# Optimization experiments

Hardware: AMD Instinct MI355X
Metric: run time of the kernel (lower is better)

## Reference

```python
import jax, jax.numpy as jnp
import numpy as np

IMG, P, CIN, D, K, L, H, FF, B = 512, 32, 3, 256, 8192, 6, 8, 1024, 32
GRID = IMG // P  # 16
DH = D // H
EPS = 1e-5


def _ln(x, w, b):
    m = x.mean(-1, keepdims=True)
    v = ((x - m) ** 2).mean(-1, keepdims=True)
    return (x - m) / jnp.sqrt(v + EPS) * w + b


def _mha(x, wqkv, bqkv, wo, bo):
    # x: (S, Bt, D) -- axis 0 is the attention axis (torch batch_first=False quirk)
    S, Bt, _ = x.shape
    qkv = x @ wqkv.T + bqkv
    q, k, v = jnp.split(qkv, 3, axis=-1)
    q = q.reshape(S, Bt, H, DH)
    k = k.reshape(S, Bt, H, DH)
    v = v.reshape(S, Bt, H, DH)
    scores = jnp.einsum('sbhd,tbhd->bhst', q, k) / jnp.sqrt(jnp.float32(DH))
    attn = jax.nn.softmax(scores, axis=-1)
    o = jnp.einsum('bhst,tbhd->sbhd', attn, v).reshape(S, Bt, D)
    return o @ wo.T + bo


def _conv_t(x, w, b, stride=2, pad=1):
    # w uses torch ConvTranspose2d layout (Cin, Cout, kH, kW)
    kH = w.shape[2]
    wf = jnp.flip(w, (2, 3)).transpose(1, 0, 2, 3)  # -> (Cout, Cin, kH, kW)
    y = jax.lax.conv_general_dilated(
        x, wf, window_strides=(1, 1),
        padding=[(kH - 1 - pad, kH - 1 - pad)] * 2,
        lhs_dilation=(stride, stride),
        dimension_numbers=('NCHW', 'OIHW', 'NCHW'))
    return y + b[None, :, None, None]


def _forward(x, patch_w, patch_b, qkv_w, qkv_b, out_w, out_b, ln1_w, ln1_b,
             ln2_w, ln2_b, ff1_w, ff1_b, ff2_w, ff2_b, lnf_w, lnf_b, codebook,
             dec_w0, dec_b0, dec_w1, dec_b1, dec_w2, dec_b2, dec_w3, dec_b3):
    # patch embedding: conv stride=patch -> (B, D, G, G) -> (B, N, D)
    h = jax.lax.conv_general_dilated(
        x, patch_w, (P, P), 'VALID',
        dimension_numbers=('NCHW', 'OIHW', 'NCHW')) + patch_b[None, :, None, None]
    h = h.reshape(h.shape[0], D, -1).transpose(0, 2, 1)  # (B, N, D)
    # torch TransformerEncoderLayer default batch_first=False: attention runs
    # over axis 0 (image batch); faithfully replicated here. Post-norm, eval
    # mode (dropout=identity), exact gelu.
    for i in range(L):
        a = _mha(h, qkv_w[i], qkv_b[i], out_w[i], out_b[i])
        h = _ln(h + a, ln1_w[i], ln1_b[i])
        f = jax.nn.gelu(h @ ff1_w[i].T + ff1_b[i], approximate=False) @ ff2_w[i].T + ff2_b[i]
        h = _ln(h + f, ln2_w[i], ln2_b[i])
    h = _ln(h, lnf_w, lnf_b)
    # vector quantization: squared-distance argmin over codebook
    flat = h.reshape(-1, D)  # (B*N, D)
    d = ((flat ** 2).sum(-1, keepdims=True)
         - 2.0 * flat @ codebook.T
         + (codebook ** 2).sum(-1))  # (B*N, K)
    idx = jnp.argmin(d, axis=1)
    q = codebook[idx].reshape(h.shape)
    e_loss = jnp.mean((jax.lax.stop_gradient(q) - h) ** 2)
    q_loss = jnp.mean((q - jax.lax.stop_gradient(h)) ** 2)
    vq_loss = q_loss + 0.25 * e_loss
    q = h + jax.lax.stop_gradient(q - h)  # straight-through
    q = q.transpose(0, 2, 1).reshape(x.shape[0], D, GRID, GRID)
    y = jax.nn.relu(_conv_t(q, dec_w0, dec_b0))
    y = jax.nn.relu(_conv_t(y, dec_w1, dec_b1))
    y = jax.nn.relu(_conv_t(y, dec_w2, dec_b2))
    x_hat = jax.nn.sigmoid(_conv_t(y, dec_w3, dec_b3))
    return x_hat, vq_loss


def setup_inputs() -> dict:
    key = jax.random.key(0)
    ks = iter(jax.random.split(key, 64))
    nrm = lambda shape, s=0.02: jax.random.normal(next(ks), shape, jnp.float32) * s
    f32 = jnp.float32
    return {
        'x': jax.random.normal(next(ks), (B, CIN, IMG, IMG), f32),
        'patch_w': nrm((D, CIN, P, P)),
        'patch_b': jnp.zeros((D,), f32),
        'qkv_w': nrm((L, 3 * D, D)),
        'qkv_b': jnp.zeros((L, 3 * D), f32),
        'out_w': nrm((L, D, D)),
        'out_b': jnp.zeros((L, D), f32),
        'ln1_w': jnp.ones((L, D), f32),
        'ln1_b': jnp.zeros((L, D), f32),
        'ln2_w': jnp.ones((L, D), f32),
        'ln2_b': jnp.zeros((L, D), f32),
        'ff1_w': nrm((L, FF, D)),
        'ff1_b': jnp.zeros((L, FF), f32),
        'ff2_w': nrm((L, D, FF)),
        'ff2_b': jnp.zeros((L, D), f32),
        'lnf_w': jnp.ones((D,), f32),
        'lnf_b': jnp.zeros((D,), f32),
        'codebook': jax.random.uniform(next(ks), (K, D), f32, -1.0 / K, 1.0 / K),
        'dec_w0': nrm((D, 256, 4, 4)),
        'dec_b0': jnp.zeros((256,), f32),
        'dec_w1': nrm((256, 128, 4, 4)),
        'dec_b1': jnp.zeros((128,), f32),
        'dec_w2': nrm((128, 64, 4, 4)),
        'dec_b2': jnp.zeros((64,), f32),
        'dec_w3': nrm((64, CIN, 4, 4)),
        'dec_b3': jnp.zeros((CIN,), f32),
    }


def reference(x, patch_w, patch_b, qkv_w, qkv_b, out_w, out_b, ln1_w, ln1_b,
              ln2_w, ln2_b, ff1_w, ff1_b, ff2_w, ff2_b, lnf_w, lnf_b, codebook,
              dec_w0, dec_b0, dec_w1, dec_b1, dec_w2, dec_b2, dec_w3, dec_b3):
    return _forward(x, patch_w, patch_b, qkv_w, qkv_b, out_w, out_b, ln1_w,
                    ln1_b, ln2_w, ln2_b, ff1_w, ff1_b, ff2_w, ff2_b, lnf_w,
                    lnf_b, codebook, dec_w0, dec_b0, dec_w1, dec_b1, dec_w2,
                    dec_b2, dec_w3, dec_b3)
```

## Files before the change

### kernel.cpp

```cpp
#include <hip/hip_runtime.h>
#include <hip/hip_bf16.h>
#include <math.h>

typedef __hip_bfloat16 bf16;
typedef unsigned int u32;
typedef unsigned long long u64;
using short8 = __attribute__((ext_vector_type(8))) short;
using f32x4  = __attribute__((ext_vector_type(4))) float;

__device__ __forceinline__ float b2f(bf16 v){ return __bfloat162float(v); }
__device__ __forceinline__ bf16  f2b(float v){ return __float2bfloat16(v); }
__device__ __forceinline__ float plo(u32 u){ return __uint_as_float(u << 16); }
__device__ __forceinline__ float phi(u32 u){ return __uint_as_float(u & 0xffff0000u); }

__device__ __forceinline__ void gld16(const void* g, void* l)
{
  __builtin_amdgcn_global_load_lds(
      (const __attribute__((address_space(1))) u32*)g,
      (__attribute__((address_space(3))) u32*)l, 16, 0, 0);
}

__global__ void k_detect(const u32* probe, int* flag)
{
  if (threadIdx.x == 0 && blockIdx.x == 0)
    *flag = (*probe == 0x3F800000u) ? 0 : 1;
}

struct PPack { const void* s[25]; u32 off[26]; };
__global__ __launch_bounds__(256) void k_convall(PPack pp, bf16* P, const int* flag)
{
  const u32 i = blockIdx.x * 256 + threadIdx.x;
  if (i >= pp.off[25]) return;
  int lo = 0, hi = 25;
  while (hi - lo > 1) { const int mid = (lo + hi) >> 1; if (i >= pp.off[mid]) lo = mid; else hi = mid; }
  const u32 j = i - pp.off[lo];
  P[i] = *flag ? ((const bf16*)pp.s[lo])[j] : f2b(((const float*)pp.s[lo])[j]);
}

__global__ __launch_bounds__(256) void k_zborder(bf16* buf, int Hp, int C, int nimg)
{
  const int per = 4 * Hp - 4;
  const int c8 = C >> 3;
  const int total = nimg * per * c8;
  const int i = blockIdx.x * 256 + threadIdx.x;
  if (i >= total) return;
  const int ch8 = i % c8;
  const int pb = i / c8;
  const int img = pb / per;
  const int b = pb - img * per;
  int y, x;
  if (b < Hp) { y = 0; x = b; }
  else if (b < 2 * Hp) { y = Hp - 1; x = b - Hp; }
  else {
    const int r = b - 2 * Hp;
    const int side = r / (Hp - 2);
    y = 1 + r - side * (Hp - 2);
    x = side ? (Hp - 1) : 0;
  }
  uint4 z = {0, 0, 0, 0};
  *reinterpret_cast<uint4*>(buf + (((size_t)img * Hp + y) * Hp + x) * C + ch8 * 8) = z;
}

__global__ __launch_bounds__(128) void k_im2col(const void* x, bf16* A, const int* flag)
{
  const int m = blockIdx.y;
  const int k8 = blockIdx.x * 128 + threadIdx.x;
  const int k = k8 * 8;
  const int b = m >> 8, n = m & 255;
  const int gy = n >> 4, gx = n & 15;
  const int c = k >> 10, r = (k >> 5) & 31, pp = k & 31;
  const size_t src = (((size_t)(b * 3 + c) * 512) + gy * 32 + r) * 512 + gx * 32 + pp;
  bf16 ov[8];
  if (*flag) {
    const bf16* xp = (const bf16*)x + src;
    #pragma unroll
    for (int i = 0; i < 8; ++i) ov[i] = xp[i];
  } else {
    const float4 v0 = *reinterpret_cast<const float4*>((const float*)x + src);
    const float4 v1 = *reinterpret_cast<const float4*>((const float*)x + src + 4);
    ov[0]=f2b(v0.x); ov[1]=f2b(v0.y); ov[2]=f2b(v0.z); ov[3]=f2b(v0.w);
    ov[4]=f2b(v1.x); ov[5]=f2b(v1.y); ov[6]=f2b(v1.z); ov[7]=f2b(v1.w);
  }
  *reinterpret_cast<uint4*>(A + (size_t)m * 3072 + k) = *reinterpret_cast<const uint4*>(ov);
}

template<int EPI, int FM, int BN, bool DB>
__global__ __launch_bounds__(256, 2) void gemm_t(
    const bf16* __restrict__ A, const bf16* __restrict__ Bw,
    const bf16* __restrict__ bias, const bf16* res, bf16* C,
    const float* __restrict__ cnorm, u64* __restrict__ ku,
    int M, int N, int K, int Kc)
{
  constexpr int BM = FM * 32;
  constexpr int FN = BN / 32;
  __shared__ alignas(16) bf16 As[DB ? 2 : 1][BM * 64];
  __shared__ alignas(16) bf16 Bs[DB ? 2 : 1][BN * 64];
  const int tid = threadIdx.x;
  const int bn = blockIdx.x * BN, bm = blockIdx.y * BM;
  const int z = blockIdx.z;
  const int kb = z * Kc;
  const int l = tid & 63, w = tid >> 6;
  const int wm = w >> 1, wn = w & 1;
  const int lg = l >> 4, lr = l & 15;
  const int sr8 = l >> 3;
  const int sch = (l & 7) ^ sr8;
  f32x4 acc[FM][FN];
  #pragma unroll
  for (int fm = 0; fm < FM; ++fm)
    #pragma unroll
    for (int fn = 0; fn < FN; ++fn) acc[fm][fn] = (f32x4){0.f, 0.f, 0.f, 0.f};

  auto stage = [&](int bb, int k0) {
    char* ab = (char*)As[bb];
    char* bp = (char*)Bs[bb];
    #pragma unroll
    for (int it = 0; it < FM; ++it) {
      const int r = w * 8 + it * 32 + sr8;
      gld16(A + (size_t)(bm + r) * K + k0 + sch * 8, ab + w * 1024 + it * 4096);
    }
    #pragma unroll
    for (int it = 0; it < BN / 32; ++it) {
      const int r = w * 8 + it * 32 + sr8;
      gld16(Bw + (size_t)(bn + r) * K + k0 + sch * 8, bp + w * 1024 + it * 4096);
    }
  };
  auto compute = [&](int bb) {
    const char* ab = (const char*)As[bb];
    const char* bp = (const char*)Bs[bb];
    #pragma unroll
    for (int ks = 0; ks < 2; ++ks) {
      short8 af[FM], bfr[FN];
      #pragma unroll
      for (int fm = 0; fm < FM; ++fm) {
        const int r = wm * (FM * 16) + fm * 16 + lr;
        af[fm] = *reinterpret_cast<const short8*>(ab + r * 128 + (((lg + ks * 4) ^ (r & 7)) * 16));
      }
      #pragma unroll
      for (int fn = 0; fn < FN; ++fn) {
        const int r = wn * (BN / 2) + fn * 16 + lr;
        bfr[fn] = *reinterpret_cast<const short8*>(bp + r * 128 + (((lg + ks * 4) ^ (r & 7)) * 16));
      }
      #pragma unroll
      for (int fm = 0; fm < FM; ++fm)
        #pragma unroll
        for (int fn = 0; fn < FN; ++fn)
          acc[fm][fn] = __builtin_amdgcn_mfma_f32_16x16x32_bf16(af[fm], bfr[fn], acc[fm][fn], 0, 0, 0);
    }
  };

  const int nt = Kc >> 6;
  if (DB) {
    stage(0, kb);
    __syncthreads();
    for (int t = 0; t < nt; ++t) {
      const int cur = t & 1;
      if (t + 1 < nt) stage(cur ^ 1, kb + ((t + 1) << 6));
      compute(cur);
      __syncthreads();
    }
  } else {
    for (int t = 0; t < nt; ++t) {
      if (t) __syncthreads();
      stage(0, kb + (t << 6));
      __syncthreads();
      compute(0);
    }
  }

  if (EPI == 3) {
    __shared__ u64 skey[BM][2];
    float cn[FN];
    #pragma unroll
    for (int fn = 0; fn < FN; ++fn) cn[fn] = cnorm[bn + wn * (BN / 2) + fn * 16 + lr];
    #pragma unroll
    for (int fm = 0; fm < FM; ++fm) {
      #pragma unroll
      for (int r = 0; r < 4; ++r) {
        u64 best = ~0ull;
        #pragma unroll
        for (int fn = 0; fn < FN; ++fn) {
          const int col = bn + wn * (BN / 2) + fn * 16 + lr;
          const float d = cn[fn] - 2.0f * acc[fm][fn][r];
          u32 u = __float_as_uint(d);
          u = (u & 0x80000000u) ? ~u : (u | 0x80000000u);
          const u64 key = ((u64)u << 32) | (u32)col;
          best = key < best ? key : best;
        }
        #pragma unroll
        for (int mk = 1; mk < 16; mk <<= 1) {
          const u64 o = __shfl_xor(best, mk, 64);
          best = o < best ? o : best;
        }
        if (lr == 0) skey[wm * (FM * 16) + fm * 16 + lg * 4 + r][wn] = best;
      }
    }
    __syncthreads();
    if (tid < BM) {
      const u64 a = skey[tid][0], b = skey[tid][1];
      ku[(size_t)blockIdx.x * M + bm + tid] = a < b ? a : b;
    }
  } else if (EPI == 4) {
    #pragma unroll
    for (int fm = 0; fm < FM; ++fm) {
      const int m0 = bm + wm * (FM * 16) + fm * 16 + lg * 4;
      #pragma unroll
      for (int fn = 0; fn < FN; ++fn) {
        const int n = bn + wn * (BN / 2) + fn * 16 + lr;
        #pragma unroll
        for (int r = 0; r < 4; ++r)
          C[((size_t)z * M + m0 + r) * N + n] = f2b(acc[fm][fn][r]);
      }
    }
  } else {
    #pragma unroll
    for (int fm = 0; fm < FM; ++fm) {
      const int m0 = bm + wm * (FM * 16) + fm * 16 + lg * 4;
      #pragma unroll
      for (int fn = 0; fn < FN; ++fn) {
        const int n = bn + wn * (BN / 2) + fn * 16 + lr;
        const float bs = b2f(bias[n]);
        #pragma unroll
        for (int r = 0; r < 4; ++r) {
          float v = acc[fm][fn][r] + bs;
          if (EPI == 1) v = 0.5f * v * (1.0f + erff(v * 0.70710678118654752f));
          if (EPI == 2) v += b2f(res[(size_t)(m0 + r) * N + n]);
          C[(size_t)(m0 + r) * N + n] = f2b(v);
        }
      }
    }
  }
}

template<bool DOLN>
__global__ __launch_bounds__(256) void k_lnred(
    const bf16* __restrict__ Pf, const bf16* __restrict__ bias,
    const bf16* res, const bf16* __restrict__ lw, const bf16* __restrict__ lb,
    bf16* h, int kc)
{
  __shared__ float red[256];
  __shared__ float stat[2];
  const int row = blockIdx.x, d = threadIdx.x;
  float s = 0.f;
  for (int z = 0; z < kc; ++z) s += b2f(Pf[((size_t)z * 8192 + row) * 256 + d]);
  s += b2f(bias[d]);
  if (res) s += b2f(res[(size_t)row * 256 + d]);
  if (!DOLN) { h[(size_t)row * 256 + d] = f2b(s); return; }
  red[d] = s;
  __syncthreads();
  for (int off = 128; off > 0; off >>= 1) {
    if (d < off) red[d] += red[d + off];
    __syncthreads();
  }
  if (d == 0) stat[0] = red[0] * (1.0f / 256.0f);
  __syncthreads();
  const float m = stat[0];
  red[d] = (s - m) * (s - m);
  __syncthreads();
  for (int off = 128; off > 0; off >>= 1) {
    if (d < off) red[d] += red[d + off];
    __syncthreads();
  }
  if (d == 0) stat[1] = 1.0f / sqrtf(red[0] * (1.0f / 256.0f) + 1e-5f);
  __syncthreads();
  h[(size_t)row * 256 + d] = f2b((s - m) * stat[1] * b2f(lw[d]) + b2f(lb[d]));
}

__global__ __launch_bounds__(256) void k_vqmerge(
    const u64* __restrict__ ku, int* __restrict__ idx, int M, int NB)
{
  const int r = blockIdx.x * 256 + threadIdx.x;
  if (r >= M) return;
  u64 best = ku[r];
  for (int nb = 1; nb < NB; ++nb) {
    const u64 k = ku[(size_t)nb * M + r];
    best = k < best ? k : best;
  }
  idx[r] = (int)(best & 0xFFFFFFFFull);
}

__global__ __launch_bounds__(256) void k_cnorm(const bf16* __restrict__ cb, float* __restrict__ cn)
{
  const int j = blockIdx.x * 256 + threadIdx.x;
  const u32* p = (const u32*)(cb + (size_t)j * 256);
  float s = 0.f;
  for (int k = 0; k < 128; ++k) {
    const u32 v = p[k];
    const float a = plo(v), b = phi(v);
    s += a * a + b * b;
  }
  cn[j] = s;
}

__global__ __launch_bounds__(256) void k_ln(
    bf16* h, const bf16* w, const bf16* b)
{
  __shared__ float red[256];
  __shared__ float stat[2];
  const int row = blockIdx.x, d = threadIdx.x;
  const size_t base = (size_t)row * 256;
  const float x = b2f(h[base + d]);
  red[d] = x;
  __syncthreads();
  for (int off = 128; off > 0; off >>= 1) {
    if (d < off) red[d] += red[d + off];
    __syncthreads();
  }
  if (d == 0) stat[0] = red[0] * (1.0f / 256.0f);
  __syncthreads();
  const float m = stat[0];
  red[d] = (x - m) * (x - m);
  __syncthreads();
  for (int off = 128; off > 0; off >>= 1) {
    if (d < off) red[d] += red[d + off];
    __syncthreads();
  }
  if (d == 0) stat[1] = 1.0f / sqrtf(red[0] * (1.0f / 256.0f) + 1e-5f);
  __syncthreads();
  h[base + d] = f2b((x - m) * stat[1] * b2f(w[d]) + b2f(b[d]));
}

__global__ __launch_bounds__(256) void k_attn(
    const bf16* __restrict__ qkv, bf16* __restrict__ o)
{
  __shared__ float qs[32][33], ks[32][33], vs[32][33], ps[32][33];
  __shared__ float rs[32];
  const int bt = blockIdx.x, hd = blockIdx.y;
  const int tid = threadIdx.x;
  #pragma unroll
  for (int e = 0; e < 2; ++e) {
    const int i = tid + 256 * e;
    if (i < 384) {
      const int plane = i >> 7;
      const int rem = i & 127;
      const int s = rem >> 2, c4 = rem & 3;
      const uint4 v = *reinterpret_cast<const uint4*>(
          qkv + (size_t)(s * 256 + bt) * 768 + plane * 256 + hd * 32 + c4 * 8);
      float* dst = (plane == 0 ? &qs[s][0] : plane == 1 ? &ks[s][0] : &vs[s][0]) + c4 * 8;
      dst[0]=plo(v.x); dst[1]=phi(v.x); dst[2]=plo(v.y); dst[3]=phi(v.y);
      dst[4]=plo(v.z); dst[5]=phi(v.z); dst[6]=plo(v.w); dst[7]=phi(v.w);
    }
  }
  __syncthreads();
  const int s = tid >> 3, j = tid & 7;
  float sc[4];
  #pragma unroll
  for (int e = 0; e < 4; ++e) {
    const int t = j + 8 * e;
    float v = 0.f;
    #pragma unroll
    for (int dd = 0; dd < 32; ++dd) v += qs[s][dd] * ks[t][dd];
    sc[e] = v * 0.17677669529663687f;
  }
  float mx = fmaxf(fmaxf(sc[0], sc[1]), fmaxf(sc[2], sc[3]));
  #pragma unroll
  for (int mk = 1; mk < 8; mk <<= 1) mx = fmaxf(mx, __shfl_xor(mx, mk, 64));
  float sm = 0.f; float ex[4];
  #pragma unroll
  for (int e = 0; e < 4; ++e) { ex[e] = expf(sc[e] - mx); sm += ex[e]; }
  #pragma unroll
  for (int mk = 1; mk < 8; mk <<= 1) sm += __shfl_xor(sm, mk, 64);
  #pragma unroll
  for (int e = 0; e < 4; ++e) ps[s][j + 8 * e] = ex[e];
  if (j == 0) rs[s] = 1.0f / sm;
  __syncthreads();
  const float rinv = rs[s];
  float av[4];
  #pragma unroll
  for (int e = 0; e < 4; ++e) {
    const int dd = j * 4 + e;
    float acc = 0.f;
    #pragma unroll
    for (int t = 0; t < 32; ++t) acc += ps[s][t] * vs[t][dd];
    av[e] = acc * rinv;
  }
  alignas(8) bf16 ov[4];
  #pragma unroll
  for (int e = 0; e < 4; ++e) ov[e] = f2b(av[e]);
  *reinterpret_cast<ushort4*>(o + (size_t)(s * 256 + bt) * 256 + hd * 32 + j * 4) =
      *reinterpret_cast<const ushort4*>(ov);
}

__global__ __launch_bounds__(256) void k_gather(
    const bf16* h, const bf16* cb, const int* idx, bf16* a0, float* lsum)
{
  __shared__ float red[256];
  const int row = blockIdx.x, d = threadIdx.x;
  const int code = idx[row] & 8191;
  const float q = b2f(cb[(size_t)code * 256 + d]);
  const float x = b2f(h[(size_t)row * 256 + d]);
  red[d] = (q - x) * (q - x);
  __syncthreads();
  for (int off = 128; off > 0; off >>= 1) {
    if (d < off) red[d] += red[d + off];
    __syncthreads();
  }
  if (d == 0) lsum[row] = red[0];
  const int b = row >> 8, n = row & 255;
  const int y = n >> 4, xc = n & 15;
  a0[(((size_t)b * 18 + y + 1) * 18 + (xc + 1)) * 256 + d] = f2b(q);
}

__global__ __launch_bounds__(256) void k_loss(const float* lsum, float* out)
{
  __shared__ float red[256];
  const int tid = threadIdx.x;
  float v = 0.f;
  for (int i = 0; i < 32; ++i) v += lsum[tid + 256 * i];
  red[tid] = v;
  __syncthreads();
  for (int off = 128; off > 0; off >>= 1) {
    if (tid < off) red[tid] += red[tid + off];
    __syncthreads();
  }
  if (tid == 0)
    out[0] = red[0] * (1.25f / 2097152.0f);
}

__global__ __launch_bounds__(256) void k_wtrans(
    const bf16* __restrict__ w, bf16* __restrict__ wt,
    int Cin, int lCin, int CoutR, int CoutP)
{
  const int K = Cin << 2;
  const int total = 4 * CoutP * K;
  const int i = blockIdx.x * 256 + threadIdx.x;
  if (i >= total) return;
  const int p = i / (CoutP * K);
  const int rem = i - p * (CoutP * K);
  const int co = rem / K;
  const int k = rem - co * K;
  const int tap = k >> lCin, ci = k - (tap << lCin);
  const int py = p >> 1, px = p & 1, ty = tap >> 1, tx = tap & 1;
  bf16 v = f2b(0.f);
  if (co < CoutR)
    v = w[(((size_t)ci * CoutR + co) * 4 + py + 2 * ty) * 4 + px + 2 * tx];
  wt[i] = v;
}

__global__ __launch_bounds__(256, 2) void convt64(
    const bf16* __restrict__ in, const bf16* __restrict__ Wt,
    const bf16* __restrict__ bias, bf16* __restrict__ outp,
    int H, int lH, int Cin, int lCin, int Cout)
{
  __shared__ alignas(16) bf16 As[2][128 * 64];
  __shared__ alignas(16) bf16 Bs[2][64 * 64];
  const int tid = threadIdx.x;
  const int pz = blockIdx.z;
  const int py = pz >> 1, px = pz & 1;
  const int K = Cin << 2;
  const int bn = blockIdx.x * 64, bm = blockIdx.y * 128;
  const bf16* Bw = Wt + (size_t)pz * Cout * K;
  const int l = tid & 63, w = tid >> 6;
  const int wm = w >> 1, wn = w & 1;
  const int lg = l >> 4, lr = l & 15;
  const int sr8 = l >> 3;
  const int sch = (l & 7) ^ sr8;
  const int Hp = H + 2;
  f32x4 acc[4][2];
  #pragma unroll
  for (int fm = 0; fm < 4; ++fm)
    #pragma unroll
    for (int fn = 0; fn < 2; ++fn) acc[fm][fn] = (f32x4){0.f, 0.f, 0.f, 0.f};

  size_t pixbase[4];
  #pragma unroll
  for (int it = 0; it < 4; ++it) {
    const int m = bm + w * 8 + it * 32 + sr8;
    const int b = m >> (2 * lH);
    const int rem = m & ((1 << (2 * lH)) - 1);
    const int jj = rem >> lH, ii = rem & (H - 1);
    pixbase[it] = ((size_t)(b * Hp + jj) * Hp + ii);
  }

  auto stage = [&](int bb, int k0) {
    char* ab = (char*)As[bb];
    char* bp = (char*)Bs[bb];
    const int tap = k0 >> lCin;
    const int ty = tap >> 1, tx = tap & 1;
    const int sy = (1 - py) + (1 - ty);
    const int sx = (1 - px) + (1 - tx);
    const int ci0 = (k0 - (tap << lCin)) + sch * 8;
    #pragma unroll
    for (int it = 0; it < 4; ++it)
      gld16(in + (pixbase[it] + (size_t)sy * Hp + sx) * Cin + ci0,
            ab + w * 1024 + it * 4096);
    #pragma unroll
    for (int it = 0; it < 2; ++it) {
      const int r = w * 8 + it * 32 + sr8;
      gld16(Bw + (size_t)(bn + r) * K + k0 + sch * 8, bp + w * 1024 + it * 4096);
    }
  };

  const int nt = K >> 6;
  stage(0, 0);
  __syncthreads();
  for (int t = 0; t < nt; ++t) {
    const int cur = t & 1;
    if (t + 1 < nt) stage(cur ^ 1, (t + 1) << 6);
    const char* ab = (const char*)As[cur];
    const char* bb = (const char*)Bs[cur];
    #pragma unroll
    for (int ks = 0; ks < 2; ++ks) {
      short8 af[4], bfr[2];
      #pragma unroll
      for (int fm = 0; fm < 4; ++fm) {
        const int r = wm * 64 + fm * 16 + lr;
        af[fm] = *reinterpret_cast<const short8*>(ab + r * 128 + (((lg + ks * 4) ^ (r & 7)) * 16));
      }
      #pragma unroll
      for (int fn = 0; fn < 2; ++fn) {
        const int r = wn * 32 + fn * 16 + lr;
        bfr[fn] = *reinterpret_cast<const short8*>(bb + r * 128 + (((lg + ks * 4) ^ (r & 7)) * 16));
      }
      #pragma unroll
      for (int fm = 0; fm < 4; ++fm)
        #pragma unroll
        for (int fn = 0; fn < 2; ++fn)
          acc[fm][fn] = __builtin_amdgcn_mfma_f32_16x16x32_bf16(af[fm], bfr[fn], acc[fm][fn], 0, 0, 0);
    }
    __syncthreads();
  }

  const int Ho = 2 * H, Hop = Ho + 2;
  #pragma unroll
  for (int fm = 0; fm < 4; ++fm) {
    const int m0 = bm + wm * 64 + fm * 16 + lg * 4;
    #pragma unroll
    for (int fn = 0; fn < 2; ++fn) {
      const int n = bn + wn * 32 + fn * 16 + lr;
      #pragma unroll
      for (int r = 0; r < 4; ++r) {
        const int m = m0 + r;
        const int b = m >> (2 * lH);
        const int rem = m & ((1 << (2 * lH)) - 1);
        const int jj = rem >> lH, ii = rem & (H - 1);
        const int oy = 2 * jj + (1 - py), ox = 2 * ii + (1 - px);
        const float v = fmaxf(acc[fm][fn][r] + b2f(bias[n]), 0.f);
        outp[((size_t)(b * Hop + oy + 1) * Hop + ox + 1) * Cout + n] = f2b(v);
      }
    }
  }
}

__global__ __launch_bounds__(256) void k_dec3(
    const bf16* __restrict__ a3, const bf16* __restrict__ wt3,
    const bf16* __restrict__ bias, float* __restrict__ xhat, int chunkBase)
{
  __shared__ float wl[3][264];
  const int tid = threadIdx.x;
  const int pz = blockIdx.y;
  const int py = pz >> 1, px = pz & 1;
  for (int i = tid; i < 768; i += 256) {
    const int co = i >> 8, k = i & 255;
    wl[co][k] = b2f(wt3[(pz * 3 + co) * 256 + k]);
  }
  __syncthreads();
  const int b = blockIdx.z;
  const int p = blockIdx.x * 64 + (tid >> 2);
  const int jj = p >> 7, ii = p & 127;
  const int ch4 = tid & 3;
  float a0 = 0.f, a1 = 0.f, a2 = 0.f;
  #pragma unroll
  for (int ty = 0; ty < 2; ++ty) {
    #pragma unroll
    for (int tx = 0; tx < 2; ++tx) {
      const int sy = (1 - py) + (1 - ty), sx = (1 - px) + (1 - tx);
      const int tap = ty * 2 + tx;
      const u32* ip = (const u32*)(a3 + ((size_t)(b * 130 + jj + sy) * 130 + ii + sx) * 64) + ch4 * 8;
      const float* w0 = &wl[0][tap * 64 + ch4 * 16];
      const float* w1 = &wl[1][tap * 64 + ch4 * 16];
      const float* w2 = &wl[2][tap * 64 + ch4 * 16];
      #pragma unroll
      for (int kk = 0; kk < 8; ++kk) {
        const u32 v = ip[kk];
        const float e0 = plo(v), e1 = phi(v);
        a0 += e0 * w0[2 * kk] + e1 * w0[2 * kk + 1];
        a1 += e0 * w1[2 * kk] + e1 * w1[2 * kk + 1];
        a2 += e0 * w2[2 * kk] + e1 * w2[2 * kk + 1];
      }
    }
  }
  a0 += __shfl_xor(a0, 1, 64); a0 += __shfl_xor(a0, 2, 64);
  a1 += __shfl_xor(a1, 1, 64); a1 += __shfl_xor(a1, 2, 64);
  a2 += __shfl_xor(a2, 1, 64); a2 += __shfl_xor(a2, 2, 64);
  if (ch4 < 3) {
    const float av = ch4 == 0 ? a0 : (ch4 == 1 ? a1 : a2);
    const int oy = 2 * jj + (1 - py), ox = 2 * ii + (1 - px);
    const float t = av + b2f(bias[ch4]);
    xhat[(((size_t)(chunkBase + b) * 3 + ch4) * 256 + oy) * 256 + ox] =
        1.0f / (1.0f + expf(-t));
  }
}

extern "C" void kernel_launch(void* const* d_in, const int* in_sizes, int n_in,
                              void* d_out, int out_size, void* d_ws, size_t ws_size,
                              hipStream_t stream)
{
  float* xhat = (float*)d_out;
  float* lossout = xhat + (out_size - 1);

  const size_t NEED = 130195456;
  if (ws_size < NEED) return;

  char* ws = (char*)d_ws;
  int*   flag  = (int*)  (ws + 0);
  float* lsum  = (float*)(ws + 1024);
  int*   idx   = (int*)  (ws + 65536);
  u64*   ku    = (u64*)  (ws + 131072);
  bf16*  P     = (bf16*) (ws + 8519680);
  bf16*  WT    = (bf16*) (ws + 27262976);
  float* cnorm = (float*)(ws + 30900224);
  bf16*  hbuf  = (bf16*) (ws + 31457280);
  bf16*  A_im  = (bf16*) (ws + 35651584);
  bf16*  qkvb  = (bf16*) (ws + 35651584);
  bf16*  obuf  = (bf16*) (ws + 48234496);
  bf16*  ffb   = (bf16*) (ws + 52428800);
  bf16*  Pfb   = (bf16*) (ws + 85983232);
  bf16*  a0    = (bf16*) (ws + 35651584);
  bf16*  a1    = (bf16*) (ws + 40960000);
  bf16*  a2    = (bf16*) (ws + 59899904);
  bf16*  a3    = (bf16*) (ws + 95584256);

  k_detect<<<1, 64, 0, stream>>>((const u32*)d_in[7], flag);

  size_t poff[26]; poff[1] = 0;
  for (int i = 2; i <= 25; ++i) poff[i] = poff[i - 1] + (size_t)in_sizes[i - 1];
  const size_t ptotal = poff[25] + (size_t)in_sizes[25];
  PPack pp;
  for (int i = 0; i < 25; ++i) { pp.s[i] = d_in[i + 1]; pp.off[i] = (u32)poff[i + 1]; }
  pp.off[25] = (u32)ptotal;
  k_convall<<<(int)((ptotal + 255) / 256), 256, 0, stream>>>(pp, P, flag);

  const bf16 *patch_w = P + poff[1],  *patch_b = P + poff[2];
  const bf16 *qkv_w   = P + poff[3],  *qkv_b   = P + poff[4];
  const bf16 *out_w   = P + poff[5],  *out_b   = P + poff[6];
  const bf16 *ln1_w   = P + poff[7],  *ln1_b   = P + poff[8];
  const bf16 *ln2_w   = P + poff[9],  *ln2_b   = P + poff[10];
  const bf16 *ff1_w   = P + poff[11], *ff1_b   = P + poff[12];
  const bf16 *ff2_w   = P + poff[13], *ff2_b   = P + poff[14];
  const bf16 *lnf_w   = P + poff[15], *lnf_b   = P + poff[16];
  const bf16 *codebook= P + poff[17];
  const bf16 *dec_w0  = P + poff[18], *dec_b0  = P + poff[19];
  const bf16 *dec_w1  = P + poff[20], *dec_b1  = P + poff[21];
  const bf16 *dec_w2  = P + poff[22], *dec_b2  = P + poff[23];
  const bf16 *dec_w3  = P + poff[24], *dec_b3  = P + poff[25];

  bf16* wt0 = WT;
  bf16* wt1 = wt0 + 1048576;
  bf16* wt2 = wt1 + 524288;
  bf16* wt3 = wt2 + 131072;
  k_wtrans<<<(1048576 + 255) / 256, 256, 0, stream>>>(dec_w0, wt0, 256, 8, 256, 256);
  k_wtrans<<<(524288 + 255) / 256, 256, 0, stream>>>(dec_w1, wt1, 256, 8, 128, 128);
  k_wtrans<<<(131072 + 255) / 256, 256, 0, stream>>>(dec_w2, wt2, 128, 7, 64, 64);
  k_wtrans<<<(3072 + 255) / 256, 256, 0, stream>>>(dec_w3, wt3, 64, 6, 3, 3);
  k_cnorm<<<32, 256, 0, stream>>>(codebook, cnorm);

  k_im2col<<<dim3(3, 8192), 128, 0, stream>>>(d_in[0], A_im, flag);
  gemm_t<4, 2, 128, true><<<dim3(2, 128, 4), 256, 0, stream>>>(
      A_im, patch_w, nullptr, nullptr, Pfb, nullptr, nullptr, 8192, 256, 3072, 768);
  k_lnred<false><<<8192, 256, 0, stream>>>(
      Pfb, patch_b, nullptr, nullptr, nullptr, hbuf, 4);

  for (int l = 0; l < 6; ++l) {
    gemm_t<0, 2, 256, false><<<dim3(3, 128, 1), 256, 0, stream>>>(
        hbuf, qkv_w + (size_t)l * 768 * 256, qkv_b + l * 768, nullptr, qkvb,
        nullptr, nullptr, 8192, 768, 256, 256);
    k_attn<<<dim3(256, 8), 256, 0, stream>>>(qkvb, obuf);
    gemm_t<2, 2, 128, false><<<dim3(2, 128, 1), 256, 0, stream>>>(
        obuf, out_w + (size_t)l * 256 * 256, out_b + l * 256, hbuf, hbuf,
        nullptr, nullptr, 8192, 256, 256, 256);
    k_ln<<<8192, 256, 0, stream>>>(hbuf, ln1_w + l * 256, ln1_b + l * 256);
    gemm_t<1, 2, 256, false><<<dim3(4, 128, 1), 256, 0, stream>>>(
        hbuf, ff1_w + (size_t)l * 1024 * 256, ff1_b + l * 1024, nullptr, ffb,
        nullptr, nullptr, 8192, 1024, 256, 256);
    gemm_t<4, 2, 128, false><<<dim3(2, 128, 4), 256, 0, stream>>>(
        ffb, ff2_w + (size_t)l * 256 * 1024, nullptr, nullptr, Pfb,
        nullptr, nullptr, 8192, 256, 1024, 256);
    k_lnred<true><<<8192, 256, 0, stream>>>(
        Pfb, ff2_b + l * 256, hbuf, ln2_w + l * 256, ln2_b + l * 256, hbuf, 4);
  }
  k_ln<<<8192, 256, 0, stream>>>(hbuf, lnf_w, lnf_b);

  gemm_t<3, 2, 256, false><<<dim3(32, 128, 1), 256, 0, stream>>>(
      hbuf, codebook, nullptr, nullptr, nullptr, cnorm, ku, 8192, 8192, 256, 256);
  k_vqmerge<<<32, 256, 0, stream>>>(ku, idx, 8192, 32);

  k_zborder<<<(32 * 68 * 32 + 255) / 256, 256, 0, stream>>>(a0, 18, 256, 32);
  k_gather<<<8192, 256, 0, stream>>>(hbuf, codebook, idx, a0, lsum);
  k_loss<<<1, 256, 0, stream>>>(lsum, lossout);
  k_zborder<<<(32 * 132 * 32 + 255) / 256, 256, 0, stream>>>(a1, 34, 256, 32);
  k_zborder<<<(32 * 260 * 16 + 255) / 256, 256, 0, stream>>>(a2, 66, 128, 32);
  k_zborder<<<(16 * 516 * 8 + 255) / 256, 256, 0, stream>>>(a3, 130, 64, 16);

  convt64<<<dim3(4, 64, 4), 256, 0, stream>>>(a0, wt0, dec_b0, a1, 16, 4, 256, 8, 256);
  convt64<<<dim3(2, 256, 4), 256, 0, stream>>>(a1, wt1, dec_b1, a2, 32, 5, 256, 8, 128);
  for (int c = 0; c < 2; ++c) {
    const bf16* a2c = a2 + (size_t)c * 16 * 66 * 66 * 128;
    convt64<<<dim3(1, 512, 4), 256, 0, stream>>>(a2c, wt2, dec_b2, a3, 64, 6, 128, 7, 64);
    k_dec3<<<dim3(256, 4, 16), 256, 0, stream>>>(a3, wt3, dec_b3, xhat, c * 16);
  }
}
```

Baseline: 1.002 ms.

## Fuse QKV projection, attention, output projection and LayerNorm into one kernel

Replaces the per-layer QKV GEMM, attention kernel, output-projection GEMM and LN1 kernel with a single kernel. Each block owns one patch position's 32 sequence rows, keeps them in LDS, computes QKV with MFMA, does the attention for all heads, then applies the output projection, residual add and LayerNorm before writing hbuf. This removes the qkv and attention-output round trips through global memory and three launches per layer. In exchange it launches only 256 blocks at one block per CU, and each block re-streams the full weight matrices with little overlap, so occupancy and latency hiding may suffer. LayerNorm variance now uses E[x^2]-m^2 instead of a two-pass computation.

```diff
diff --git a/kernel.cpp b/kernel.cpp
--- a/kernel.cpp
+++ b/kernel.cpp
@@ -231,6 +231,241 @@
   }
 }
 
+__global__ __launch_bounds__(256, 1) void k_fat1(
+    bf16* __restrict__ hbuf,
+    const bf16* __restrict__ Wqkv, const bf16* __restrict__ Bqkv,
+    const bf16* __restrict__ Wo, const bf16* __restrict__ Bo,
+    const bf16* __restrict__ lw, const bf16* __restrict__ lb)
+{
+  __shared__ alignas(16) bf16 hs[32 * 256];
+  __shared__ alignas(16) bf16 ao[32 * 256];
+  __shared__ alignas(16) bf16 astage[128 * 64];
+  __shared__ bf16 att[3 * 9216];
+  __shared__ float ps[32][33];
+  __shared__ float rs[32];
+  __shared__ float psum[32][4], psq[32][4];
+  __shared__ float mstat[32], istat[32];
+
+  const int bt = blockIdx.x;
+  const int tid = threadIdx.x;
+  const int l = tid & 63, w = tid >> 6;
+  const int lg = l >> 4, lr = l & 15;
+  const int sr8 = l >> 3;
+  const int sch = (l & 7) ^ sr8;
+  char* hsb = (char*)hs;
+  char* aob = (char*)ao;
+  char* asb = (char*)astage;
+
+  #pragma unroll
+  for (int call = 0; call < 4; ++call) {
+    const int id = call * 256 + tid;
+    const int s = id >> 5, within = id & 31;
+    const int grp = within >> 3, c = within & 7;
+    gld16(hbuf + (size_t)(s * 256 + bt) * 256 + grp * 64 + ((c ^ (s & 7)) * 8),
+          hsb + call * 4096 + w * 1024);
+  }
+
+  for (int at = 0; at < 6; ++at) {
+    f32x4 acc[2][2];
+    #pragma unroll
+    for (int fm = 0; fm < 2; ++fm)
+      #pragma unroll
+      for (int fn = 0; fn < 2; ++fn) acc[fm][fn] = (f32x4){0.f, 0.f, 0.f, 0.f};
+    for (int kst = 0; kst < 4; ++kst) {
+      __syncthreads();
+      #pragma unroll
+      for (int it = 0; it < 4; ++it) {
+        const int r = w * 8 + it * 32 + sr8;
+        gld16(Wqkv + (size_t)(at * 128 + r) * 256 + kst * 64 + sch * 8,
+              asb + w * 1024 + it * 4096);
+      }
+      __syncthreads();
+      #pragma unroll
+      for (int ks = 0; ks < 2; ++ks) {
+        short8 af[2], bfr[2];
+        #pragma unroll
+        for (int fm = 0; fm < 2; ++fm) {
+          const int r = w * 32 + fm * 16 + lr;
+          af[fm] = *reinterpret_cast<const short8*>(asb + r * 128 + (((lg + ks * 4) ^ (r & 7)) * 16));
+        }
+        #pragma unroll
+        for (int fn = 0; fn < 2; ++fn) {
+          const int sr = fn * 16 + lr;
+          bfr[fn] = *reinterpret_cast<const short8*>(hsb + sr * 512 + kst * 128 + (((lg + ks * 4) ^ (sr & 7)) * 16));
+        }
+        #pragma unroll
+        for (int fm = 0; fm < 2; ++fm)
+          #pragma unroll
+          for (int fn = 0; fn < 2; ++fn)
+            acc[fm][fn] = __builtin_amdgcn_mfma_f32_16x16x32_bf16(af[fm], bfr[fn], acc[fm][fn], 0, 0, 0);
+      }
+    }
+    #pragma unroll
+    for (int fm = 0; fm < 2; ++fm) {
+      #pragma unroll
+      for (int fn = 0; fn < 2; ++fn) {
+        const int s = fn * 16 + lr;
+        #pragma unroll
+        for (int r = 0; r < 4; ++r) {
+          const int n = at * 128 + w * 32 + fm * 16 + lg * 4 + r;
+          const int p = n >> 8, rem = n & 255;
+          att[p * 9216 + (rem >> 5) * 1152 + s * 36 + (rem & 31)] =
+              f2b(acc[fm][fn][r] + b2f(Bqkv[n]));
+        }
+      }
+    }
+  }
+  __syncthreads();
+
+  const int s_a = tid >> 3, j_a = tid & 7;
+  for (int hd = 0; hd < 8; ++hd) {
+    const bf16* qrow = att + hd * 1152 + s_a * 36;
+    float sc[4];
+    #pragma unroll
+    for (int e = 0; e < 4; ++e) {
+      const int t = j_a + 8 * e;
+      const bf16* krow = att + 9216 + hd * 1152 + t * 36;
+      float v = 0.f;
+      #pragma unroll
+      for (int dd = 0; dd < 32; ++dd) v += b2f(qrow[dd]) * b2f(krow[dd]);
+      sc[e] = v * 0.17677669529663687f;
+    }
+    float mx = fmaxf(fmaxf(sc[0], sc[1]), fmaxf(sc[2], sc[3]));
+    #pragma unroll
+    for (int mk = 1; mk < 8; mk <<= 1) mx = fmaxf(mx, __shfl_xor(mx, mk, 64));
+    float sm = 0.f; float ex[4];
+    #pragma unroll
+    for (int e = 0; e < 4; ++e) { ex[e] = expf(sc[e] - mx); sm += ex[e]; }
+    #pragma unroll
+    for (int mk = 1; mk < 8; mk <<= 1) sm += __shfl_xor(sm, mk, 64);
+    #pragma unroll
+    for (int e = 0; e < 4; ++e) ps[s_a][j_a + 8 * e] = ex[e];
+    if (j_a == 0) rs[s_a] = 1.0f / sm;
+    __syncthreads();
+    const float rinv = rs[s_a];
+    float av[4];
+    #pragma unroll
+    for (int e = 0; e < 4; ++e) {
+      const int dd = j_a * 4 + e;
+      float a = 0.f;
+      #pragma unroll
+      for (int t = 0; t < 32; ++t)
+        a += ps[s_a][t] * b2f(att[2 * 9216 + hd * 1152 + t * 36 + dd]);
+      av[e] = a * rinv;
+    }
+    alignas(8) bf16 ov[4];
+    #pragma unroll
+    for (int e = 0; e < 4; ++e) ov[e] = f2b(av[e]);
+    const int clog = (hd & 1) * 4 + (j_a >> 1);
+    *reinterpret_cast<ushort4*>(aob + s_a * 512 + (hd >> 1) * 128 +
+        ((clog ^ (s_a & 7)) * 16) + (j_a & 1) * 8) =
+        *reinterpret_cast<const ushort4*>(ov);
+    __syncthreads();
+  }
+
+  float vals[2][2][2][4];
+  for (int at = 0; at < 2; ++at) {
+    f32x4 acc[2][2];
+    #pragma unroll
+    for (int fm = 0; fm < 2; ++fm)
+      #pragma unroll
+      for (int fn = 0; fn < 2; ++fn) acc[fm][fn] = (f32x4){0.f, 0.f, 0.f, 0.f};
+    for (int kst = 0; kst < 4; ++kst) {
+      __syncthreads();
+      #pragma unroll
+      for (int it = 0; it < 4; ++it) {
+        const int r = w * 8 + it * 32 + sr8;
+        gld16(Wo + (size_t)(at * 128 + r) * 256 + kst * 64 + sch * 8,
+              asb + w * 1024 + it * 4096);
+      }
+      __syncthreads();
+      #pragma unroll
+      for (int ks = 0; ks < 2; ++ks) {
+        short8 af[2], bfr[2];
+        #pragma unroll
+        for (int fm = 0; fm < 2; ++fm) {
+          const int r = w * 32 + fm * 16 + lr;
+          af[fm] = *reinterpret_cast<const short8*>(asb + r * 128 + (((lg + ks * 4) ^ (r & 7)) * 16));
+        }
+        #pragma unroll
+        for (int fn = 0; fn < 2; ++fn) {
+          const int sr = fn * 16 + lr;
+          bfr[fn] = *reinterpret_cast<const short8*>(aob + sr * 512 + kst * 128 + (((lg + ks * 4) ^ (sr & 7)) * 16));
+        }
+        #pragma unroll
+        for (int fm = 0; fm < 2; ++fm)
+          #pragma unroll
+          for (int fn = 0; fn < 2; ++fn)
+            acc[fm][fn] = __builtin_amdgcn_mfma_f32_16x16x32_bf16(af[fm], bfr[fn], acc[fm][fn], 0, 0, 0);
+      }
+    }
+    #pragma unroll
+    for (int fm = 0; fm < 2; ++fm)
+      #pragma unroll
+      for (int fn = 0; fn < 2; ++fn)
+        #pragma unroll
+        for (int r = 0; r < 4; ++r) vals[at][fm][fn][r] = acc[fm][fn][r];
+  }
+
+  float s1[2] = {0.f, 0.f}, s2[2] = {0.f, 0.f};
+  #pragma unroll
+  for (int at = 0; at < 2; ++at) {
+    #pragma unroll
+    for (int fm = 0; fm < 2; ++fm) {
+      const int n4 = at * 128 + w * 32 + fm * 16 + lg * 4;
+      #pragma unroll
+      for (int fn = 0; fn < 2; ++fn) {
+        const int s = fn * 16 + lr;
+        const ushort4 hr = *reinterpret_cast<const ushort4*>(
+            hsb + s * 512 + (n4 >> 6) * 128 + ((((n4 >> 3) & 7) ^ (s & 7)) * 16) + (n4 & 7) * 2);
+        const bf16* hb = reinterpret_cast<const bf16*>(&hr);
+        #pragma unroll
+        for (int r = 0; r < 4; ++r) {
+          const float v = vals[at][fm][fn][r] + b2f(Bo[n4 + r]) + b2f(hb[r]);
+          vals[at][fm][fn][r] = v;
+          s1[fn] += v;
+          s2[fn] += v * v;
+        }
+      }
+    }
+  }
+  #pragma unroll
+  for (int fn = 0; fn < 2; ++fn) {
+    float a = s1[fn], b = s2[fn];
+    a += __shfl_xor(a, 16, 64); a += __shfl_xor(a, 32, 64);
+    b += __shfl_xor(b, 16, 64); b += __shfl_xor(b, 32, 64);
+    if (lg == 0) { psum[fn * 16 + lr][w] = a; psq[fn * 16 + lr][w] = b; }
+  }
+  __syncthreads();
+  if (tid < 32) {
+    float sa = 0.f, sb = 0.f;
+    #pragma unroll
+    for (int k = 0; k < 4; ++k) { sa += psum[tid][k]; sb += psq[tid][k]; }
+    const float m = sa * (1.0f / 256.0f);
+    mstat[tid] = m;
+    istat[tid] = 1.0f / sqrtf(sb * (1.0f / 256.0f) - m * m + 1e-5f);
+  }
+  __syncthreads();
+  #pragma unroll
+  for (int at = 0; at < 2; ++at) {
+    #pragma unroll
+    for (int fm = 0; fm < 2; ++fm) {
+      const int n4 = at * 128 + w * 32 + fm * 16 + lg * 4;
+      #pragma unroll
+      for (int fn = 0; fn < 2; ++fn) {
+        const int s = fn * 16 + lr;
+        const float m = mstat[s], inv = istat[s];
+        alignas(8) bf16 ov[4];
+        #pragma unroll
+        for (int r = 0; r < 4; ++r)
+          ov[r] = f2b((vals[at][fm][fn][r] - m) * inv * b2f(lw[n4 + r]) + b2f(lb[n4 + r]));
+        *reinterpret_cast<ushort4*>(hbuf + (size_t)(s * 256 + bt) * 256 + n4) =
+            *reinterpret_cast<const ushort4*>(ov);
+      }
+    }
+  }
+}
+
 template<bool DOLN>
 __global__ __launch_bounds__(256) void k_lnred(
     const bf16* __restrict__ Pf, const bf16* __restrict__ bias,
@@ -317,67 +552,6 @@
   if (d == 0) stat[1] = 1.0f / sqrtf(red[0] * (1.0f / 256.0f) + 1e-5f);
   __syncthreads();
   h[base + d] = f2b((x - m) * stat[1] * b2f(w[d]) + b2f(b[d]));
-}
-
-__global__ __launch_bounds__(256) void k_attn(
-    const bf16* __restrict__ qkv, bf16* __restrict__ o)
-{
-  __shared__ float qs[32][33], ks[32][33], vs[32][33], ps[32][33];
-  __shared__ float rs[32];
-  const int bt = blockIdx.x, hd = blockIdx.y;
-  const int tid = threadIdx.x;
-  #pragma unroll
-  for (int e = 0; e < 2; ++e) {
-    const int i = tid + 256 * e;
-    if (i < 384) {
-      const int plane = i >> 7;
-      const int rem = i & 127;
-      const int s = rem >> 2, c4 = rem & 3;
-      const uint4 v = *reinterpret_cast<const uint4*>(
-          qkv + (size_t)(s * 256 + bt) * 768 + plane * 256 + hd * 32 + c4 * 8);
-      float* dst = (plane == 0 ? &qs[s][0] : plane == 1 ? &ks[s][0] : &vs[s][0]) + c4 * 8;
-      dst[0]=plo(v.x); dst[1]=phi(v.x); dst[2]=plo(v.y); dst[3]=phi(v.y);
-      dst[4]=plo(v.z); dst[5]=phi(v.z); dst[6]=plo(v.w); dst[7]=phi(v.w);
-    }
-  }
-  __syncthreads();
-  const int s = tid >> 3, j = tid & 7;
-  float sc[4];
-  #pragma unroll
-  for (int e = 0; e < 4; ++e) {
-    const int t = j + 8 * e;
-    float v = 0.f;
-    #pragma unroll
-    for (int dd = 0; dd < 32; ++dd) v += qs[s][dd] * ks[t][dd];
-    sc[e] = v * 0.17677669529663687f;
-  }
-  float mx = fmaxf(fmaxf(sc[0], sc[1]), fmaxf(sc[2], sc[3]));
-  #pragma unroll
-  for (int mk = 1; mk < 8; mk <<= 1) mx = fmaxf(mx, __shfl_xor(mx, mk, 64));
-  float sm = 0.f; float ex[4];
-  #pragma unroll
-  for (int e = 0; e < 4; ++e) { ex[e] = expf(sc[e] - mx); sm += ex[e]; }
-  #pragma unroll
-  for (int mk = 1; mk < 8; mk <<= 1) sm += __shfl_xor(sm, mk, 64);
-  #pragma unroll
-  for (int e = 0; e < 4; ++e) ps[s][j + 8 * e] = ex[e];
-  if (j == 0) rs[s] = 1.0f / sm;
-  __syncthreads();
-  const float rinv = rs[s];
-  float av[4];
-  #pragma unroll
-  for (int e = 0; e < 4; ++e) {
-    const int dd = j * 4 + e;
-    float acc = 0.f;
-    #pragma unroll
-    for (int t = 0; t < 32; ++t) acc += ps[s][t] * vs[t][dd];
-    av[e] = acc * rinv;
-  }
-  alignas(8) bf16 ov[4];
-  #pragma unroll
-  for (int e = 0; e < 4; ++e) ov[e] = f2b(av[e]);
-  *reinterpret_cast<ushort4*>(o + (size_t)(s * 256 + bt) * 256 + hd * 32 + j * 4) =
-      *reinterpret_cast<const ushort4*>(ov);
 }
 
 __global__ __launch_bounds__(256) void k_gather(
@@ -611,8 +785,6 @@
   float* cnorm = (float*)(ws + 30900224);
   bf16*  hbuf  = (bf16*) (ws + 31457280);
   bf16*  A_im  = (bf16*) (ws + 35651584);
-  bf16*  qkvb  = (bf16*) (ws + 35651584);
-  bf16*  obuf  = (bf16*) (ws + 48234496);
   bf16*  ffb   = (bf16*) (ws + 52428800);
   bf16*  Pfb   = (bf16*) (ws + 85983232);
   bf16*  a0    = (bf16*) (ws + 35651584);
@@ -661,14 +833,10 @@
       Pfb, patch_b, nullptr, nullptr, nullptr, hbuf, 4);
 
   for (int l = 0; l < 6; ++l) {
-    gemm_t<0, 2, 256, false><<<dim3(3, 128, 1), 256, 0, stream>>>(
-        hbuf, qkv_w + (size_t)l * 768 * 256, qkv_b + l * 768, nullptr, qkvb,
-        nullptr, nullptr, 8192, 768, 256, 256);
-    k_attn<<<dim3(256, 8), 256, 0, stream>>>(qkvb, obuf);
-    gemm_t<2, 2, 128, false><<<dim3(2, 128, 1), 256, 0, stream>>>(
-        obuf, out_w + (size_t)l * 256 * 256, out_b + l * 256, hbuf, hbuf,
-        nullptr, nullptr, 8192, 256, 256, 256);
-    k_ln<<<8192, 256, 0, stream>>>(hbuf, ln1_w + l * 256, ln1_b + l * 256);
+    k_fat1<<<256, 256, 0, stream>>>(
+        hbuf, qkv_w + (size_t)l * 768 * 256, qkv_b + l * 768,
+        out_w + (size_t)l * 256 * 256, out_b + l * 256,
+        ln1_w + l * 256, ln1_b + l * 256);
     gemm_t<1, 2, 256, false><<<dim3(4, 128, 1), 256, 0, stream>>>(
         hbuf, ff1_w + (size_t)l * 1024 * 256, ff1_b + l * 1024, nullptr, ffb,
         nullptr, nullptr, 8192, 1024, 256, 256);
```

Result: faster. 973.9 us (median of 2 runs) (-2.8%).
